# Performance work log

Hardware: AMD Instinct MI355X
Metric: run time of the kernel (lower is better)

The kernel has to match this reference:

```python
import jax, jax.numpy as jnp
import numpy as np

N = 50000
E = 1600000
IN_C = 512
HID = 128
HEADS = 8
OUT_C = 64
NEG_SLOPE = 0.2


def setup_inputs() -> dict:
    key = jax.random.key(0)
    ks = jax.random.split(key, 10)
    x = jax.random.normal(ks[0], (N, IN_C), dtype=jnp.float32)
    edge_index = jax.random.randint(ks[1], (2, E), 0, N, dtype=jnp.int32)
    s1 = 1.0 / np.sqrt(IN_C)
    W1 = jax.random.uniform(ks[2], (IN_C, HEADS * HID), jnp.float32, -s1, s1)
    att_src1 = jax.random.normal(ks[3], (HEADS, HID), jnp.float32) * 0.1
    att_dst1 = jax.random.normal(ks[4], (HEADS, HID), jnp.float32) * 0.1
    b1 = jnp.zeros((HEADS * HID,), jnp.float32)
    s2 = 1.0 / np.sqrt(HEADS * HID)
    W2 = jax.random.uniform(ks[5], (HEADS * HID, OUT_C), jnp.float32, -s2, s2)
    att_src2 = jax.random.normal(ks[6], (1, OUT_C), jnp.float32) * 0.1
    att_dst2 = jax.random.normal(ks[7], (1, OUT_C), jnp.float32) * 0.1
    b2 = jnp.zeros((OUT_C,), jnp.float32)
    return {"x": x, "edge_index": edge_index, "W1": W1, "att_src1": att_src1,
            "att_dst1": att_dst1, "b1": b1, "W2": W2, "att_src2": att_src2,
            "att_dst2": att_dst2, "b2": b2}


def gat_conv(x, src, dst, W, a_src, a_dst, b, heads, ch, concat):
    n = x.shape[0]
    h = (x @ W).reshape(n, heads, ch)                      # [N,H,C]
    alpha_s = jnp.einsum('nhc,hc->nh', h, a_src)           # [N,H]
    alpha_d = jnp.einsum('nhc,hc->nh', h, a_dst)           # [N,H]
    logits = jax.nn.leaky_relu(alpha_s[src] + alpha_d[dst], NEG_SLOPE)  # [E,H]
    # segment softmax over edges grouped by destination node
    m = jax.ops.segment_max(logits, dst, num_segments=n)
    e = jnp.exp(logits - m[dst])
    z = jax.ops.segment_sum(e, dst, num_segments=n)
    alpha = e / z[dst]                                     # [E,H]
    msg = h[src] * alpha[:, :, None]                       # [E,H,C]
    out = jax.ops.segment_sum(msg, dst, num_segments=n)    # [N,H,C]
    out = out.reshape(n, heads * ch) if concat else out.mean(axis=1)
    return out + b


def reference(x, edge_index, W1, att_src1, att_dst1, b1, W2, att_src2, att_dst2, b2):
    n = x.shape[0]
    loops = jnp.arange(n, dtype=edge_index.dtype)
    src = jnp.concatenate([edge_index[0], loops])
    dst = jnp.concatenate([edge_index[1], loops])
    h = gat_conv(x, src, dst, W1, att_src1, att_dst1, b1, HEADS, HID, True)
    h = jax.nn.elu(h)
    out = gat_conv(h, src, dst, W2, att_src2, att_dst2, b2, 1, OUT_C, False)
    return jax.nn.log_softmax(out, axis=1)
```

## Files before the change

kernel.cpp:

```cpp
#include <hip/hip_runtime.h>
#include <hip/hip_bf16.h>

#define NN 50000
#define EE 1600000
#define ET (EE + NN)
#define HEADS 8
#define HID 128
#define INC 512
#define H1C (HEADS * HID)
#define OUTC 64
#define NEG_SLOPE 0.2f

typedef unsigned short u16;
typedef unsigned int u32;
typedef unsigned char u8;
typedef __attribute__((ext_vector_type(8))) __bf16 bf16x8;
typedef __attribute__((ext_vector_type(4))) float f32x4;
typedef __attribute__((ext_vector_type(2))) float f32x2;
typedef __attribute__((ext_vector_type(4))) u32 u32x4;

__device__ __forceinline__ float lrelu(float x) { return x > 0.f ? x : NEG_SLOPE * x; }
__device__ __forceinline__ float us2f(u16 u) { return __uint_as_float(((u32)u) << 16); }
__device__ __forceinline__ u16 f2bs(float f) {
    u32 u = __float_as_uint(f);
    u += 0x7fffu + ((u >> 16) & 1u);
    return (u16)(u >> 16);
}

__device__ __forceinline__ void gload_lds16(const void* g, void* lds) {
    __builtin_amdgcn_global_load_lds((const __attribute__((address_space(1))) void*)g,
                                     (__attribute__((address_space(3))) void*)lds, 16, 0, 0);
}

__global__ __launch_bounds__(256) void cvt_x_k(const float* __restrict__ x, u16* __restrict__ xb) {
    int i = blockIdx.x * 256 + threadIdx.x;
    float4 v = ((const float4*)x)[i];
    ushort4 o; o.x = f2bs(v.x); o.y = f2bs(v.y); o.z = f2bs(v.z); o.w = f2bs(v.w);
    ((ushort4*)xb)[i] = o;
}

__global__ __launch_bounds__(256) void cvt_w1t_k(const float* __restrict__ W, u16* __restrict__ Wt) {
    int idx = blockIdx.x * 256 + threadIdx.x;
    int n = idx >> 9, k = idx & 511;
    Wt[idx] = f2bs(W[k * 1024 + n]);
}

__global__ __launch_bounds__(256) void cvt_w2t_k(const float* __restrict__ W, u16* __restrict__ Wt) {
    int idx = blockIdx.x * 256 + threadIdx.x;
    int n = idx >> 10, k = idx & 1023;
    Wt[idx] = f2bs(W[k * 64 + n]);
}

__global__ __launch_bounds__(256) void hist_k(const int* __restrict__ ei, int* __restrict__ cnt) {
    int e = blockIdx.x * 256 + threadIdx.x;
    if (e >= ET) return;
    int d = (e < EE) ? ei[EE + e] : (e - EE);
    atomicAdd(&cnt[d], 1);
}

__global__ __launch_bounds__(256) void scan1_k(const int* __restrict__ cnt,
                                               int* __restrict__ startp, int* __restrict__ bsum) {
    __shared__ int ws[8];
    int tid = threadIdx.x;
    int i = blockIdx.x * 256 + tid;
    int v = (i < NN) ? cnt[i] : 0;
    int lane = tid & 63, w = tid >> 6;
    int x = v;
#pragma unroll
    for (int off = 1; off < 64; off <<= 1) { int t = __shfl_up(x, off); if (lane >= off) x += t; }
    if (lane == 63) ws[w] = x;
    __syncthreads();
    if (tid == 0) { int s = 0; for (int k = 0; k < 4; ++k) { int t = ws[k]; ws[k] = s; s += t; } }
    __syncthreads();
    x += ws[w];
    if (i < NN) startp[i] = x - v;
    if (tid == 255) bsum[blockIdx.x] = x;
}

__global__ __launch_bounds__(256) void scan2_k(const int* __restrict__ bsum,
                                               int* __restrict__ boff, int nb) {
    __shared__ int ws[8];
    int tid = threadIdx.x;
    int v = (tid < nb) ? bsum[tid] : 0;
    int lane = tid & 63, w = tid >> 6;
    int x = v;
#pragma unroll
    for (int off = 1; off < 64; off <<= 1) { int t = __shfl_up(x, off); if (lane >= off) x += t; }
    if (lane == 63) ws[w] = x;
    __syncthreads();
    if (tid == 0) { int s = 0; for (int k = 0; k < 4; ++k) { int t = ws[k]; ws[k] = s; s += t; } }
    __syncthreads();
    x += ws[w];
    if (tid < nb) boff[tid] = x - v;
}

__global__ __launch_bounds__(256) void scan3_k(int* __restrict__ startp, const int* __restrict__ boff) {
    int i = blockIdx.x * 256 + threadIdx.x;
    if (i < NN) startp[i] += boff[blockIdx.x];
}

__global__ __launch_bounds__(256) void scatter_k(const int* __restrict__ ei,
                                                 const int* __restrict__ start,
                                                 int* __restrict__ cursor,
                                                 int* __restrict__ csr_src) {
    int e = blockIdx.x * 256 + threadIdx.x;
    if (e >= ET) return;
    int s, d;
    if (e < EE) { s = ei[e]; d = ei[EE + e]; }
    else        { s = e - EE; d = e - EE; }
    int pos = start[d] + atomicAdd(&cursor[d], 1);
    csr_src[pos] = s;
}

__device__ __forceinline__ void stf(float* p, float v) { *p = v; }
__device__ __forceinline__ void stf(u16* p, float v)   { *p = f2bs(v); }
__device__ __forceinline__ void stf(u8* p, float v) {
    u32 pk = __builtin_amdgcn_cvt_pk_fp8_f32(v, v, 0, false);
    *p = (u8)(pk & 0xff);
}

template<int BM, int BN, typename TC, bool FUSE, int SWZ>
__global__ __launch_bounds__(256) void mgemm_k(const u16* __restrict__ A,
                                               const u16* __restrict__ Bt,
                                               TC* __restrict__ C,
                                               const float* __restrict__ att_s,
                                               const float* __restrict__ att_d,
                                               float* __restrict__ as_o,
                                               float* __restrict__ ad_o,
                                               int M, int K, int Ncol, int NH) {
    __shared__ __align__(16) u16 As[BM * 64];
    __shared__ __align__(16) u16 Bs[BN * 64];
    __shared__ float asL[2][BM], adL[2][BM];
    int tid = threadIdx.x;
    int wid = tid >> 6, lane = tid & 63;

    int wg = blockIdx.x;
    if (SWZ) { int q = gridDim.x >> 3; wg = (blockIdx.x & 7) * q + (blockIdx.x >> 3); }
    int nbn = Ncol / BN;
    int bm_i = wg / nbn, bn_i = wg % nbn;
    int bm = bm_i * BM, bn = bn_i * BN;

    constexpr int WN = BN / 2;
    constexpr int FM = 4;
    constexpr int FN = WN / 16;
    constexpr int TA = BM * 64 * 2 / 1024;
    constexpr int TB = BN * 64 * 2 / 1024;
    int wr = wid >> 1, wc = wid & 1;

    f32x4 acc[FM][FN] = {};

    for (int k0 = 0; k0 < K; k0 += 64) {
#pragma unroll
        for (int i = 0; i < TA / 4; ++i) {
            int t = wid * (TA / 4) + i;
            int o = t * 1024 + lane * 16;
            int m = o >> 7;
            int b = o & 127;
            int kb = b ^ ((m & 7) << 4);
            int gm = bm + m; if (gm >= M) gm = M - 1;
            gload_lds16(A + ((size_t)gm * K + k0 + (kb >> 1)), (char*)As + t * 1024);
        }
#pragma unroll
        for (int i = 0; i < TB / 4; ++i) {
            int t = wid * (TB / 4) + i;
            int o = t * 1024 + lane * 16;
            int n = o >> 7;
            int b = o & 127;
            int kb = b ^ ((n & 7) << 4);
            gload_lds16(Bt + ((size_t)(bn + n) * K + k0 + (kb >> 1)), (char*)Bs + t * 1024);
        }
        __syncthreads();
        int g = lane >> 4, r = lane & 15;
#pragma unroll
        for (int kh = 0; kh < 2; ++kh) {
            int kbb = g * 16 + kh * 64;
            bf16x8 af[FM], bfr[FN];
#pragma unroll
            for (int fm = 0; fm < FM; ++fm) {
                int m = wr * 64 + fm * 16 + r;
                af[fm] = *(const bf16x8*)((const char*)As + m * 128 + (kbb ^ ((m & 7) << 4)));
            }
#pragma unroll
            for (int fn = 0; fn < FN; ++fn) {
                int n = wc * WN + fn * 16 + r;
                bfr[fn] = *(const bf16x8*)((const char*)Bs + n * 128 + (kbb ^ ((n & 7) << 4)));
            }
#pragma unroll
            for (int fm = 0; fm < FM; ++fm)
#pragma unroll
                for (int fn = 0; fn < FN; ++fn)
                    acc[fm][fn] = __builtin_amdgcn_mfma_f32_16x16x32_bf16(af[fm], bfr[fn], acc[fm][fn], 0, 0, 0);
        }
        __syncthreads();
    }
#pragma unroll
    for (int fm = 0; fm < FM; ++fm)
#pragma unroll
        for (int fn = 0; fn < FN; ++fn)
#pragma unroll
            for (int rr = 0; rr < 4; ++rr) {
                int gm = bm + wr * 64 + fm * 16 + (lane >> 4) * 4 + rr;
                int gn = bn + wc * WN + fn * 16 + (lane & 15);
                if (gm < M) stf(&C[(size_t)gm * Ncol + gn], acc[fm][fn][rr]);
            }

    if constexpr (FUSE) {
        float asv[FN], adv[FN];
#pragma unroll
        for (int fn = 0; fn < FN; ++fn) {
            int c = bn + wc * WN + fn * 16 + (lane & 15);
            asv[fn] = att_s[c]; adv[fn] = att_d[c];
        }
#pragma unroll
        for (int fm = 0; fm < FM; ++fm)
#pragma unroll
            for (int rr = 0; rr < 4; ++rr) {
                float ps = 0.f, pd = 0.f;
#pragma unroll
                for (int fn = 0; fn < FN; ++fn) {
                    ps += acc[fm][fn][rr] * asv[fn];
                    pd += acc[fm][fn][rr] * adv[fn];
                }
#pragma unroll
                for (int off = 1; off < 16; off <<= 1) {
                    ps += __shfl_xor(ps, off);
                    pd += __shfl_xor(pd, off);
                }
                if ((lane & 15) == 0) {
                    int rl = wr * 64 + fm * 16 + (lane >> 4) * 4 + rr;
                    asL[wc][rl] = ps; adL[wc][rl] = pd;
                }
            }
        __syncthreads();
        if (tid < BM) {
            int gm = bm + tid;
            if (gm < M) {
                as_o[(size_t)gm * NH + bn_i] = asL[0][tid] + asL[1][tid];
                ad_o[(size_t)gm * NH + bn_i] = adL[0][tid] + adL[1][tid];
            }
        }
    }
}

__global__ __launch_bounds__(256) void agg1_k(const u8* __restrict__ h1,
                                              const float* __restrict__ as1,
                                              const float* __restrict__ ad1,
                                              const int* __restrict__ start,
                                              const int* __restrict__ cnt,
                                              const int* __restrict__ csr_src,
                                              const float* __restrict__ b1,
                                              u16* __restrict__ out1) {
    int n = blockIdx.x;
    int tid = threadIdx.x;
    int s0 = start[n], deg = cnt[n];
    __shared__ float mred[256], zred[256];
    __shared__ float m_sh[8], rz_sh[8], ad_sh[8];
    __shared__ int src_sh[32];
    __shared__ float al_sh[32][8];
    __shared__ float comb[3][64][17];

    if (tid < 8) ad_sh[tid] = ad1[n * 8 + tid];
    __syncthreads();

    int h = tid & 7;
    float adh = ad_sh[h];
    float m = -1e30f, z = 0.f;
    for (int e = (tid >> 3); e < deg; e += 32) {
        int s = csr_src[s0 + e];
        float l = lrelu(as1[s * 8 + h] + adh);
        if (l > m) { z = z * __expf(m - l) + 1.f; m = l; }
        else       { z += __expf(l - m); }
    }
    mred[tid] = m; zred[tid] = z;
    __syncthreads();
#pragma unroll
    for (int off = 128; off >= 8; off >>= 1) {
        if (tid < off) {
            float m1 = mred[tid], z1 = zred[tid];
            float m2 = mred[tid + off], z2 = zred[tid + off];
            float mm = fmaxf(m1, m2);
            mred[tid] = mm;
            zred[tid] = z1 * __expf(m1 - mm) + z2 * __expf(m2 - mm);
        }
        __syncthreads();
    }
    if (tid < 8) { m_sh[tid] = mred[tid]; rz_sh[tid] = 1.f / zred[tid]; }
    __syncthreads();

    int l = tid & 63, grp = tid >> 6;
    int myh = l >> 3;
    float acc[16] = {};
    const char* h1b = (const char*)h1;
    for (int e0 = 0; e0 < deg; e0 += 32) {
        int ne = min(32, deg - e0);
        if (tid < ne) src_sh[tid] = csr_src[s0 + e0 + tid];
        __syncthreads();
        if (tid < ne * 8) {
            int ee = tid >> 3, hh = tid & 7;
            int s = src_sh[ee];
            al_sh[ee][hh] = __expf(lrelu(as1[s * 8 + hh] + ad_sh[hh]) - m_sh[hh]) * rz_sh[hh];
        }
        __syncthreads();
        int j = grp;
        if (j < ne) {
            u32x4 v = *(const u32x4*)(h1b + (size_t)src_sh[j] * 1024 + l * 16);
            while (true) {
                int jn = j + 4;
                bool more = jn < ne;
                u32x4 vn;
                if (more) vn = *(const u32x4*)(h1b + (size_t)src_sh[jn] * 1024 + l * 16);
                float al = al_sh[j][myh];
#pragma unroll
                for (int w = 0; w < 4; ++w) {
                    u32 word = v[w];
                    f32x2 p0 = __builtin_amdgcn_cvt_pk_f32_fp8(word, false);
                    f32x2 p1 = __builtin_amdgcn_cvt_pk_f32_fp8(word, true);
                    acc[w * 4 + 0] += al * p0.x;
                    acc[w * 4 + 1] += al * p0.y;
                    acc[w * 4 + 2] += al * p1.x;
                    acc[w * 4 + 3] += al * p1.y;
                }
                if (!more) break;
                v = vn; j = jn;
            }
        }
        __syncthreads();
    }
    if (grp) {
#pragma unroll
        for (int c = 0; c < 16; ++c) comb[grp - 1][l][c] = acc[c];
    }
    __syncthreads();
    if (!grp) {
        int cbase = l * 16;
        float o[16];
#pragma unroll
        for (int c = 0; c < 16; ++c) {
            float zz = acc[c] + comb[0][l][c] + comb[1][l][c] + comb[2][l][c] + b1[cbase + c];
            o[c] = zz > 0.f ? zz : (__expf(zz) - 1.f);
        }
        u32x4 pk0, pk1;
#pragma unroll
        for (int i = 0; i < 4; ++i) {
            pk0[i] = (u32)f2bs(o[2 * i])     | ((u32)f2bs(o[2 * i + 1]) << 16);
            pk1[i] = (u32)f2bs(o[8 + 2 * i]) | ((u32)f2bs(o[9 + 2 * i]) << 16);
        }
        char* dst = (char*)out1 + (size_t)n * 2048 + l * 32;
        __builtin_nontemporal_store(pk0, (u32x4*)dst);
        __builtin_nontemporal_store(pk1, (u32x4*)(dst + 16));
    }
}

__global__ __launch_bounds__(256) void agg2_k(const u16* __restrict__ h2,
                                              const float* __restrict__ as2,
                                              const float* __restrict__ ad2,
                                              const int* __restrict__ start,
                                              const int* __restrict__ cnt,
                                              const int* __restrict__ csr_src,
                                              const float* __restrict__ b2,
                                              float* __restrict__ out) {
    int n = blockIdx.x * 4 + (threadIdx.x >> 6);
    int lane = threadIdx.x & 63;
    if (n >= NN) return;
    int s0 = start[n], deg = cnt[n];
    float adn = ad2[n];

    float pm = -1e30f, pz = 0.f;
    for (int e = lane; e < deg; e += 64) {
        int s = csr_src[s0 + e];
        float l = lrelu(as2[s] + adn);
        if (l > pm) { pz = pz * __expf(pm - l) + 1.f; pm = l; }
        else        { pz += __expf(l - pm); }
    }
#pragma unroll
    for (int off = 32; off; off >>= 1) {
        float m2 = __shfl_xor(pm, off), z2 = __shfl_xor(pz, off);
        float mm = fmaxf(pm, m2);
        pz = pz * __expf(pm - mm) + z2 * __expf(m2 - mm);
        pm = mm;
    }
    float rz = 1.f / pz;

    int half = lane >> 5, l = lane & 31;
    float a0 = 0.f, a1 = 0.f;
    int j = half;
    if (j < deg) {
        int s = csr_src[s0 + j];
        float asv = as2[s];
        u32 v = *(const u32*)(h2 + (size_t)s * 64 + l * 2);
        while (true) {
            int jn = j + 2;
            bool more = jn < deg;
            int sn; float asn; u32 vn;
            if (more) {
                sn = csr_src[s0 + jn];
                asn = as2[sn];
                vn = *(const u32*)(h2 + (size_t)sn * 64 + l * 2);
            }
            float al = __expf(lrelu(asv + adn) - pm) * rz;
            a0 += al * us2f((u16)(v & 0xffff));
            a1 += al * us2f((u16)(v >> 16));
            if (!more) break;
            asv = asn; v = vn; j = jn;
        }
    }
    a0 += __shfl_xor(a0, 32);
    a1 += __shfl_xor(a1, 32);
    float y0 = a0 + b2[2 * l], y1 = a1 + b2[2 * l + 1];

    float mm = fmaxf(y0, y1);
#pragma unroll
    for (int off = 16; off; off >>= 1) mm = fmaxf(mm, __shfl_xor(mm, off));
    float se = __expf(y0 - mm) + __expf(y1 - mm);
#pragma unroll
    for (int off = 16; off; off >>= 1) se += __shfl_xor(se, off);
    float ls = __logf(se);
    if (half == 0) {
        float2 o; o.x = y0 - mm - ls; o.y = y1 - mm - ls;
        *(float2*)(out + (size_t)n * 64 + 2 * l) = o;
    }
}

extern "C" void kernel_launch(void* const* d_in, const int* in_sizes, int n_in,
                              void* d_out, int out_size, void* d_ws, size_t ws_size,
                              hipStream_t stream) {
    const float* x     = (const float*)d_in[0];
    const int*   ei    = (const int*)d_in[1];
    const float* W1    = (const float*)d_in[2];
    const float* aw_s1 = (const float*)d_in[3];
    const float* aw_d1 = (const float*)d_in[4];
    const float* b1    = (const float*)d_in[5];
    const float* W2    = (const float*)d_in[6];
    const float* aw_s2 = (const float*)d_in[7];
    const float* aw_d2 = (const float*)d_in[8];
    const float* b2    = (const float*)d_in[9];
    float* out = (float*)d_out;

    char* ws = (char*)d_ws;
    size_t off = 0;
    auto alloc = [&](size_t bytes) -> void* {
        void* p = (void*)(ws + off);
        off += (bytes + 511) & ~(size_t)511;
        return p;
    };
    u16*   out1    = (u16*)alloc((size_t)NN * H1C * 2);
    u16*   xb      = out1;
    u8*    h1      = (u8*)alloc((size_t)NN * H1C);
    u16*   h2      = (u16*)h1;
    u16*   w1t     = (u16*)alloc((size_t)H1C * INC * 2);
    u16*   w2t     = (u16*)alloc((size_t)OUTC * H1C * 2);
    float* as1     = (float*)alloc((size_t)NN * 8 * 4);
    float* ad1     = (float*)alloc((size_t)NN * 8 * 4);
    float* as2     = (float*)alloc((size_t)NN * 4);
    float* ad2     = (float*)alloc((size_t)NN * 4);
    int*   cnt     = (int*)alloc((size_t)NN * 4);
    int*   startp  = (int*)alloc((size_t)NN * 4);
    int*   cursor  = (int*)alloc((size_t)NN * 4);
    int*   csr_src = (int*)alloc((size_t)ET * 4);
    int    nsb     = (NN + 255) / 256;
    int*   bsum    = (int*)alloc((size_t)nsb * 4);
    int*   boff    = (int*)alloc((size_t)nsb * 4);

    if (off > ws_size) return;

    hipMemsetAsync(cnt, 0, (size_t)NN * 4, stream);
    hipMemsetAsync(cursor, 0, (size_t)NN * 4, stream);

    cvt_x_k<<<(NN * INC / 4) / 256, 256, 0, stream>>>(x, xb);
    cvt_w1t_k<<<(INC * H1C) / 256, 256, 0, stream>>>(W1, w1t);
    cvt_w2t_k<<<(H1C * OUTC) / 256, 256, 0, stream>>>(W2, w2t);

    int eblk = (ET + 255) / 256;
    hist_k<<<eblk, 256, 0, stream>>>(ei, cnt);
    scan1_k<<<nsb, 256, 0, stream>>>(cnt, startp, bsum);
    scan2_k<<<1, 256, 0, stream>>>(bsum, boff, nsb);
    scan3_k<<<nsb, 256, 0, stream>>>(startp, boff);
    scatter_k<<<eblk, 256, 0, stream>>>(ei, startp, cursor, csr_src);

    int nwg1 = (H1C / 128) * ((NN + 127) / 128);
    mgemm_k<128, 128, u8, true, 1><<<nwg1, 256, 0, stream>>>(
        xb, w1t, h1, aw_s1, aw_d1, as1, ad1, NN, INC, H1C, HEADS);
    agg1_k<<<NN, 256, 0, stream>>>(h1, as1, ad1, startp, cnt, csr_src, b1, out1);

    int nwg2 = (OUTC / 64) * ((NN + 127) / 128);
    mgemm_k<128, 64, u16, true, 0><<<nwg2, 256, 0, stream>>>(
        out1, w2t, h2, aw_s2, aw_d2, as2, ad2, NN, H1C, OUTC, 1);
    agg2_k<<<(NN + 3) / 4, 256, 0, stream>>>(h2, as2, ad2, startp, cnt, csr_src, b2, out);
}
```

Baseline: 852.3 us.

## Fuse GAT softmax normalization into aggregation pass, dropping the max pass

Both aggregation kernels drop the separate pass over incoming edges that computed the running max and softmax denominator. They now compute unnormalized exp(logit) weights during the feature-gather loop, accumulate the denominator alongside, and divide once at the end. This removes a second walk over csr_src and the attention-score gathers, plus a block-wide max/sum reduction. agg1 also grows its edge chunk from 32 to 64. Without max subtraction, exp can overflow when logits are large; the current inputs keep logits small.

```diff
diff --git a/kernel.cpp b/kernel.cpp
--- a/kernel.cpp
+++ b/kernel.cpp
@@ -253,52 +253,31 @@
     int n = blockIdx.x;
     int tid = threadIdx.x;
     int s0 = start[n], deg = cnt[n];
-    __shared__ float mred[256], zred[256];
-    __shared__ float m_sh[8], rz_sh[8], ad_sh[8];
-    __shared__ int src_sh[32];
-    __shared__ float al_sh[32][8];
+    __shared__ float ad_sh[8], rz_sh[8];
+    __shared__ int src_sh[64];
+    __shared__ float al_sh[64][8];
+    __shared__ float zred[256];
     __shared__ float comb[3][64][17];
 
     if (tid < 8) ad_sh[tid] = ad1[n * 8 + tid];
-    __syncthreads();
-
-    int h = tid & 7;
-    float adh = ad_sh[h];
-    float m = -1e30f, z = 0.f;
-    for (int e = (tid >> 3); e < deg; e += 32) {
-        int s = csr_src[s0 + e];
-        float l = lrelu(as1[s * 8 + h] + adh);
-        if (l > m) { z = z * __expf(m - l) + 1.f; m = l; }
-        else       { z += __expf(l - m); }
-    }
-    mred[tid] = m; zred[tid] = z;
-    __syncthreads();
-#pragma unroll
-    for (int off = 128; off >= 8; off >>= 1) {
-        if (tid < off) {
-            float m1 = mred[tid], z1 = zred[tid];
-            float m2 = mred[tid + off], z2 = zred[tid + off];
-            float mm = fmaxf(m1, m2);
-            mred[tid] = mm;
-            zred[tid] = z1 * __expf(m1 - mm) + z2 * __expf(m2 - mm);
-        }
-        __syncthreads();
-    }
-    if (tid < 8) { m_sh[tid] = mred[tid]; rz_sh[tid] = 1.f / zred[tid]; }
     __syncthreads();
 
     int l = tid & 63, grp = tid >> 6;
     int myh = l >> 3;
     float acc[16] = {};
+    float zacc = 0.f;
     const char* h1b = (const char*)h1;
-    for (int e0 = 0; e0 < deg; e0 += 32) {
-        int ne = min(32, deg - e0);
+
+    for (int e0 = 0; e0 < deg; e0 += 64) {
+        int ne = min(64, deg - e0);
         if (tid < ne) src_sh[tid] = csr_src[s0 + e0 + tid];
         __syncthreads();
-        if (tid < ne * 8) {
-            int ee = tid >> 3, hh = tid & 7;
+        for (int i = tid; i < ne * 8; i += 256) {
+            int ee = i >> 3, hh = i & 7;
             int s = src_sh[ee];
-            al_sh[ee][hh] = __expf(lrelu(as1[s * 8 + hh] + ad_sh[hh]) - m_sh[hh]) * rz_sh[hh];
+            float al = __expf(lrelu(as1[s * 8 + hh] + ad_sh[hh]));
+            al_sh[ee][hh] = al;
+            zacc += al;
         }
         __syncthreads();
         int j = grp;
@@ -326,17 +305,29 @@
         }
         __syncthreads();
     }
+
+    zred[tid] = zacc;
+    __syncthreads();
+#pragma unroll
+    for (int off = 128; off >= 8; off >>= 1) {
+        if (tid < off) zred[tid] += zred[tid + off];
+        __syncthreads();
+    }
+    if (tid < 8) rz_sh[tid] = 1.f / zred[tid];
+    __syncthreads();
+
     if (grp) {
 #pragma unroll
         for (int c = 0; c < 16; ++c) comb[grp - 1][l][c] = acc[c];
     }
     __syncthreads();
     if (!grp) {
+        float rz = rz_sh[myh];
         int cbase = l * 16;
         float o[16];
 #pragma unroll
         for (int c = 0; c < 16; ++c) {
-            float zz = acc[c] + comb[0][l][c] + comb[1][l][c] + comb[2][l][c] + b1[cbase + c];
+            float zz = (acc[c] + comb[0][l][c] + comb[1][l][c] + comb[2][l][c]) * rz + b1[cbase + c];
             o[c] = zz > 0.f ? zz : (__expf(zz) - 1.f);
         }
         u32x4 pk0, pk1;
@@ -365,24 +356,8 @@
     int s0 = start[n], deg = cnt[n];
     float adn = ad2[n];
 
-    float pm = -1e30f, pz = 0.f;
-    for (int e = lane; e < deg; e += 64) {
-        int s = csr_src[s0 + e];
-        float l = lrelu(as2[s] + adn);
-        if (l > pm) { pz = pz * __expf(pm - l) + 1.f; pm = l; }
-        else        { pz += __expf(l - pm); }
-    }
-#pragma unroll
-    for (int off = 32; off; off >>= 1) {
-        float m2 = __shfl_xor(pm, off), z2 = __shfl_xor(pz, off);
-        float mm = fmaxf(pm, m2);
-        pz = pz * __expf(pm - mm) + z2 * __expf(m2 - mm);
-        pm = mm;
-    }
-    float rz = 1.f / pz;
-
     int half = lane >> 5, l = lane & 31;
-    float a0 = 0.f, a1 = 0.f;
+    float a0 = 0.f, a1 = 0.f, z = 0.f;
     int j = half;
     if (j < deg) {
         int s = csr_src[s0 + j];
@@ -397,7 +372,8 @@
                 asn = as2[sn];
                 vn = *(const u32*)(h2 + (size_t)sn * 64 + l * 2);
             }
-            float al = __expf(lrelu(asv + adn) - pm) * rz;
+            float al = __expf(lrelu(asv + adn));
+            z += al;
             a0 += al * us2f((u16)(v & 0xffff));
             a1 += al * us2f((u16)(v >> 16));
             if (!more) break;
@@ -406,7 +382,9 @@
     }
     a0 += __shfl_xor(a0, 32);
     a1 += __shfl_xor(a1, 32);
-    float y0 = a0 + b2[2 * l], y1 = a1 + b2[2 * l + 1];
+    z  += __shfl_xor(z, 32);
+    float rz = 1.f / z;
+    float y0 = a0 * rz + b2[2 * l], y1 = a1 * rz + b2[2 * l + 1];
 
     float mm = fmaxf(y0, y1);
 #pragma unroll
```

Measured after the change: 790.8 us. 1.08x faster.
